# Performance work log

Hardware: AMD Instinct MI355X
Metric: run time of the kernel (lower is better)

## Reference

```python
import jax, jax.numpy as jnp
import numpy as np

N, F_IN, D_OUT, H = 8192, 512, 64, 8
ALPHA = 0.2
NEG_INF = jnp.float32(-9e15)


def setup_inputs() -> dict:
    key = jax.random.key(0)
    k1, k2, k3, k4, k5 = jax.random.split(key, 5)
    x = jax.random.normal(k1, (N, F_IN), dtype=jnp.float32)
    # sparse-ish binary adjacency (avg degree ~33) with self-loops, stored dense
    adj = (jax.random.uniform(k2, (N, N)) < 0.004).astype(jnp.float32)
    adj = jnp.maximum(adj, jnp.eye(N, dtype=jnp.float32))
    W = jax.random.normal(k3, (H, F_IN, D_OUT), dtype=jnp.float32) * 0.05
    a1 = jax.random.normal(k4, (H, D_OUT), dtype=jnp.float32) * 0.05
    a2 = jax.random.normal(k5, (H, D_OUT), dtype=jnp.float32) * 0.05
    return {"x": x, "adj": adj, "W": W, "a1": a1, "a2": a2}


def reference(x, adj, W, a1, a2):
    mask = adj > 0
    outputs = []
    for h in range(H):  # fixed small head count (matches original per-head loop)
        Wh = x @ W[h]                      # [N, D]
        f1 = Wh @ a1[h]                    # [N]
        f2 = Wh @ a2[h]                    # [N]
        e = jax.nn.leaky_relu(f1[:, None] + f2[None, :], ALPHA)  # [N, N]
        att = jnp.where(mask, e, NEG_INF)
        att = jax.nn.softmax(att, axis=1)  # dropout omitted (eval mode)
        outputs.append(att @ Wh)           # [N, D]
    return jnp.concatenate(outputs, axis=1)  # [N, H*D]
```

## Files before the change

kernel.cpp:

```cpp
#include <hip/hip_runtime.h>
#include <hip/hip_bf16.h>
#include <cstdint>

#define N_NODES 8192
#define F_IN    512
#define D_O     64
#define H_N     8
#define NOUT    512
#define MAXD    512

typedef __attribute__((ext_vector_type(8))) short short8;
typedef __attribute__((ext_vector_type(4))) float f32x4;

static __device__ __forceinline__ ushort f2bf(float f) {
  union { float f; uint32_t u; } v; v.f = f;
  uint32_t r = v.u + 0x7FFFu + ((v.u >> 16) & 1u);
  return (ushort)(r >> 16);
}
static __device__ __forceinline__ float bf2f(ushort u) {
  union { uint32_t u; float f; } v; v.u = ((uint32_t)u) << 16;
  return v.f;
}

__global__ __launch_bounds__(256) void convert(const float* __restrict__ x,
                                               const float* __restrict__ W,
                                               ushort* __restrict__ xb,
                                               ushort* __restrict__ Wt) {
  const int gid    = blockIdx.x * 256 + threadIdx.x;
  const int stride = gridDim.x * 256;
  const int NQ = N_NODES * F_IN / 4;
  for (int q = gid; q < NQ; q += stride) {
    const float4 v = ((const float4*)x)[q];
    ushort4 u;
    u.x = f2bf(v.x); u.y = f2bf(v.y); u.z = f2bf(v.z); u.w = f2bf(v.w);
    ((ushort4*)xb)[q] = u;
  }
  const int NW = H_N * D_O * F_IN;
  for (int t = gid; t < NW; t += stride) {
    const int h = t >> 15, rem = t & 32767;
    const int d = rem >> 9, k = rem & 511;
    Wt[t] = f2bf(W[(size_t)h * F_IN * D_O + (size_t)k * D_O + d]);
  }
}

__global__ __launch_bounds__(256) void gemm_xw(const ushort* __restrict__ xb,
                                               const ushort* __restrict__ Wt,
                                               ushort* __restrict__ Whb) {
  __shared__ ushort As[128][40];
  __shared__ ushort Bs[128][40];

  const int tid  = threadIdx.x;
  const int lane = tid & 63;
  const int wv   = tid >> 6;
  const int wr   = wv >> 1, wc = wv & 1;
  const int r0   = blockIdx.y * 128;
  const int c0   = blockIdx.x * 128;
  const int lm   = lane & 15;
  const int lk   = (lane >> 4) * 8;

  f32x4 acc[4][4];
  #pragma unroll
  for (int m2 = 0; m2 < 4; ++m2)
    #pragma unroll
    for (int n2 = 0; n2 < 4; ++n2)
      acc[m2][n2] = (f32x4){0.f, 0.f, 0.f, 0.f};

  for (int k0 = 0; k0 < F_IN; k0 += 32) {
    __syncthreads();
    #pragma unroll
    for (int half = 0; half < 2; ++half) {
      const int cid = half * 256 + tid;
      const int row = cid >> 2, ck = (cid & 3) * 8;
      *(short8*)&As[row][ck] = *(const short8*)&xb[(size_t)(r0 + row) * F_IN + k0 + ck];
      *(short8*)&Bs[row][ck] = *(const short8*)&Wt[(size_t)(c0 + row) * F_IN + k0 + ck];
    }
    __syncthreads();

    short8 af[4], bf[4];
    #pragma unroll
    for (int m2 = 0; m2 < 4; ++m2)
      af[m2] = *(const short8*)&As[wr * 64 + m2 * 16 + lm][lk];
    #pragma unroll
    for (int n2 = 0; n2 < 4; ++n2)
      bf[n2] = *(const short8*)&Bs[wc * 64 + n2 * 16 + lm][lk];
    #pragma unroll
    for (int m2 = 0; m2 < 4; ++m2)
      #pragma unroll
      for (int n2 = 0; n2 < 4; ++n2)
        acc[m2][n2] = __builtin_amdgcn_mfma_f32_16x16x32_bf16(af[m2], bf[n2], acc[m2][n2], 0, 0, 0);
  }

  const int rowb = (lane >> 4) * 4;
  #pragma unroll
  for (int m2 = 0; m2 < 4; ++m2) {
    #pragma unroll
    for (int n2 = 0; n2 < 4; ++n2) {
      const int c     = c0 + wc * 64 + n2 * 16 + lm;
      const int rbase = r0 + wr * 64 + m2 * 16 + rowb;
      #pragma unroll
      for (int r = 0; r < 4; ++r)
        Whb[(size_t)(rbase + r) * NOUT + c] = f2bf(acc[m2][n2][r]);
    }
  }
}

__global__ __launch_bounds__(256) void f_proj(const ushort* __restrict__ Whb,
                                              const float* __restrict__ a1,
                                              const float* __restrict__ a2,
                                              float* __restrict__ f1,
                                              float* __restrict__ f2) {
  const int gw   = blockIdx.x * 4 + (threadIdx.x >> 6);
  const int lane = threadIdx.x & 63;
  const int i = gw >> 3, h = gw & 7;
  const float wv = bf2f(Whb[(size_t)i * NOUT + h * D_O + lane]);
  float v1 = wv * a1[h * D_O + lane];
  float v2 = wv * a2[h * D_O + lane];
  #pragma unroll
  for (int o = 32; o; o >>= 1) {
    v1 += __shfl_xor(v1, o);
    v2 += __shfl_xor(v2, o);
  }
  if (lane == 0) { f1[gw] = v1; f2[gw] = v2; }
}

__global__ __launch_bounds__(256) void gat_attn(const uint32_t* __restrict__ adj,
                                                const ushort* __restrict__ Whb,
                                                const float* __restrict__ f1,
                                                const float* __restrict__ f2,
                                                float* __restrict__ out) {
  const int i    = blockIdx.x;
  const int tid  = threadIdx.x;
  const int lane = tid & 63;
  const int w    = tid >> 6;

  __shared__ int   nbr[MAXD];
  __shared__ float p[MAXD][9];
  __shared__ float f1s[8], invs[8];
  __shared__ int   wsum[4];

  if (tid < 8) f1s[tid] = f1[(size_t)i * H_N + tid];

  const uint32_t* arow = adj + (size_t)i * N_NODES;
  uint32_t bits = 0;
  #pragma unroll
  for (int u = 0; u < 8; ++u) {
    const uint4 a = *(const uint4*)&arow[(u * 256 + tid) * 4];
    if (a.x) bits |= 1u << (u * 4 + 0);
    if (a.y) bits |= 1u << (u * 4 + 1);
    if (a.z) bits |= 1u << (u * 4 + 2);
    if (a.w) bits |= 1u << (u * 4 + 3);
  }
  const int cnt = __popc(bits);
  int v = cnt;
  #pragma unroll
  for (int o = 1; o < 64; o <<= 1) {
    int u = __shfl_up(v, o);
    if (lane >= o) v += u;
  }
  if (lane == 63) wsum[w] = v;
  __syncthreads();
  int base = 0, total = 0;
  #pragma unroll
  for (int ww = 0; ww < 4; ++ww) {
    int s = wsum[ww];
    if (ww < w) base += s;
    total += s;
  }
  const int deg = min(total, MAXD);
  int off = base + v - cnt;
  #pragma unroll
  for (int u = 0; u < 8; ++u)
    #pragma unroll
    for (int b = 0; b < 4; ++b)
      if (bits & (1u << (u * 4 + b))) {
        if (off < MAXD) nbr[off] = (u * 256 + tid) * 4 + b;
        ++off;
      }
  __syncthreads();

  for (int idx = tid; idx < deg * H_N; idx += 256) {
    const int n = idx >> 3, h = idx & 7;
    const int j = nbr[n];
    float l = f1s[h] + f2[(size_t)j * H_N + h];
    l = l > 0.f ? l : 0.2f * l;
    p[n][h] = l;
  }
  __syncthreads();

  #pragma unroll
  for (int hh = 0; hh < 2; ++hh) {
    const int h = w + hh * 4;
    float m = -3.0e38f;
    for (int n = lane; n < deg; n += 64) m = fmaxf(m, p[n][h]);
    #pragma unroll
    for (int o = 32; o; o >>= 1) m = fmaxf(m, __shfl_xor(m, o));
    float s = 0.f;
    for (int n = lane; n < deg; n += 64) {
      const float e = __expf(p[n][h] - m);
      p[n][h] = e;
      s += e;
    }
    #pragma unroll
    for (int o = 32; o; o >>= 1) s += __shfl_xor(s, o);
    if (lane == 0) invs[h] = 1.0f / s;
  }
  __syncthreads();

  const int h = tid >> 5;
  float acc0 = 0.f, acc1 = 0.f;
  #pragma unroll 4
  for (int n = 0; n < deg; ++n) {
    const float pv = p[n][h];
    const ushort2 u = *(const ushort2*)&Whb[(size_t)nbr[n] * NOUT + tid * 2];
    acc0 += pv * bf2f(u.x);
    acc1 += pv * bf2f(u.y);
  }
  const float inv = invs[h];
  float2 o2; o2.x = acc0 * inv; o2.y = acc1 * inv;
  *(float2*)&out[(size_t)i * NOUT + tid * 2] = o2;
}

extern "C" void kernel_launch(void* const* d_in, const int* in_sizes, int n_in,
                              void* d_out, int out_size, void* d_ws, size_t ws_size,
                              hipStream_t stream) {
  const float* x   = (const float*)d_in[0];
  const float* adj = (const float*)d_in[1];
  const float* W   = (const float*)d_in[2];
  const float* a1  = (const float*)d_in[3];
  const float* a2  = (const float*)d_in[4];
  float* out = (float*)d_out;

  ushort* Whb = (ushort*)d_ws;
  ushort* xb  = Whb + (size_t)N_NODES * NOUT;
  ushort* Wt  = xb + (size_t)N_NODES * F_IN;
  float*  f1  = (float*)(Wt + (size_t)H_N * D_O * F_IN);
  float*  f2  = f1 + (size_t)N_NODES * H_N;

  hipLaunchKernelGGL(convert, dim3(2048), dim3(256), 0, stream, x, W, xb, Wt);
  hipLaunchKernelGGL(gemm_xw, dim3(NOUT / 128, N_NODES / 128), dim3(256), 0, stream,
                     xb, Wt, Whb);
  hipLaunchKernelGGL(f_proj, dim3(N_NODES * H_N / 4), dim3(256), 0, stream,
                     Whb, a1, a2, f1, f2);
  hipLaunchKernelGGL(gat_attn, dim3(N_NODES), dim3(256), 0, stream,
                     (const uint32_t*)adj, Whb, f1, f2, out);
}
```

Baseline: 111.0 us.

## Fuse attention projections into GEMM epilogue and tile the W transpose

Folds the f1/f2 projection into the x·W GEMM epilogue, reducing each head's 64 accumulator columns with shuffles, so the separate f_proj kernel and its re-read of Wh disappear. The GEMM tiling becomes 64x128 with BK=64, which doubles the number of blocks. The W transpose in the convert kernel now goes through shared memory so its global reads are coalesced, and a larger unroll is applied to the gather loop in gat_attn. The trade-offs are a heavier epilogue and smaller tiles, which give less reuse per block.

New measurement: 98.28 us. -11.5%, faster.

```diff
diff --git a/kernel.cpp b/kernel.cpp
--- a/kernel.cpp
+++ b/kernel.cpp
@@ -9,6 +9,10 @@
 #define NOUT    512
 #define MAXD    512
 
+#define BM 64
+#define BN 128
+#define BK 64
+
 typedef __attribute__((ext_vector_type(8))) short short8;
 typedef __attribute__((ext_vector_type(4))) float f32x4;
 
@@ -26,101 +30,127 @@
                                                const float* __restrict__ W,
                                                ushort* __restrict__ xb,
                                                ushort* __restrict__ Wt) {
-  const int gid    = blockIdx.x * 256 + threadIdx.x;
-  const int stride = gridDim.x * 256;
-  const int NQ = N_NODES * F_IN / 4;
-  for (int q = gid; q < NQ; q += stride) {
-    const float4 v = ((const float4*)x)[q];
-    ushort4 u;
-    u.x = f2bf(v.x); u.y = f2bf(v.y); u.z = f2bf(v.z); u.w = f2bf(v.w);
-    ((ushort4*)xb)[q] = u;
-  }
-  const int NW = H_N * D_O * F_IN;
-  for (int t = gid; t < NW; t += stride) {
-    const int h = t >> 15, rem = t & 32767;
-    const int d = rem >> 9, k = rem & 511;
-    Wt[t] = f2bf(W[(size_t)h * F_IN * D_O + (size_t)k * D_O + d]);
-  }
-}
-
-__global__ __launch_bounds__(256) void gemm_xw(const ushort* __restrict__ xb,
-                                               const ushort* __restrict__ Wt,
-                                               ushort* __restrict__ Whb) {
-  __shared__ ushort As[128][40];
-  __shared__ ushort Bs[128][40];
+  __shared__ float Ws[64][65];
+  const int b = blockIdx.x, t = threadIdx.x;
+  if (b < 2048) {
+    const int gid = b * 256 + t;
+    #pragma unroll
+    for (int it = 0; it < 2; ++it) {
+      const int q = gid + it * 524288;
+      const float4 v = ((const float4*)x)[q];
+      ushort4 u;
+      u.x = f2bf(v.x); u.y = f2bf(v.y); u.z = f2bf(v.z); u.w = f2bf(v.w);
+      ((ushort4*)xb)[q] = u;
+    }
+  } else {
+    const int bb = b - 2048;
+    const int h = bb >> 3, kt = bb & 7;
+    const int d = t & 63, krg = (t >> 6) * 16;
+    const float* src = &W[((size_t)h * F_IN + kt * 64 + krg) * D_O + d];
+    #pragma unroll
+    for (int q = 0; q < 16; ++q)
+      Ws[krg + q][d] = src[(size_t)q * D_O];
+    __syncthreads();
+    const int d0 = t >> 2, kq = (t & 3) * 16;
+    ushort* dst = &Wt[(size_t)h * D_O * F_IN + (size_t)d0 * F_IN + kt * 64 + kq];
+    #pragma unroll
+    for (int q = 0; q < 16; ++q)
+      dst[q] = f2bf(Ws[kq + q][d0]);
+  }
+}
+
+__global__ __launch_bounds__(256) void gemm_f(const ushort* __restrict__ xb,
+                                              const ushort* __restrict__ Wt,
+                                              const float* __restrict__ a1,
+                                              const float* __restrict__ a2,
+                                              ushort* __restrict__ Whb,
+                                              float* __restrict__ f1,
+                                              float* __restrict__ f2) {
+  __shared__ ushort As[BM][BK + 8];
+  __shared__ ushort Bs[BN][BK + 8];
 
   const int tid  = threadIdx.x;
   const int lane = tid & 63;
   const int wv   = tid >> 6;
   const int wr   = wv >> 1, wc = wv & 1;
-  const int r0   = blockIdx.y * 128;
-  const int c0   = blockIdx.x * 128;
+  const int r0   = blockIdx.y * BM;
+  const int c0   = blockIdx.x * BN;
   const int lm   = lane & 15;
-  const int lk   = (lane >> 4) * 8;
-
-  f32x4 acc[4][4];
-  #pragma unroll
-  for (int m2 = 0; m2 < 4; ++m2)
+  const int lg   = lane >> 4;
+
+  f32x4 acc[2][4];
+  #pragma unroll
+  for (int m2 = 0; m2 < 2; ++m2)
     #pragma unroll
     for (int n2 = 0; n2 < 4; ++n2)
       acc[m2][n2] = (f32x4){0.f, 0.f, 0.f, 0.f};
 
-  for (int k0 = 0; k0 < F_IN; k0 += 32) {
+  for (int k0 = 0; k0 < F_IN; k0 += BK) {
     __syncthreads();
     #pragma unroll
-    for (int half = 0; half < 2; ++half) {
-      const int cid = half * 256 + tid;
-      const int row = cid >> 2, ck = (cid & 3) * 8;
+    for (int p = 0; p < 2; ++p) {
+      const int e = p * 256 + tid;
+      const int row = e >> 3, ck = (e & 7) * 8;
       *(short8*)&As[row][ck] = *(const short8*)&xb[(size_t)(r0 + row) * F_IN + k0 + ck];
+    }
+    #pragma unroll
+    for (int p = 0; p < 4; ++p) {
+      const int e = p * 256 + tid;
+      const int row = e >> 3, ck = (e & 7) * 8;
       *(short8*)&Bs[row][ck] = *(const short8*)&Wt[(size_t)(c0 + row) * F_IN + k0 + ck];
     }
     __syncthreads();
 
-    short8 af[4], bf[4];
-    #pragma unroll
-    for (int m2 = 0; m2 < 4; ++m2)
-      af[m2] = *(const short8*)&As[wr * 64 + m2 * 16 + lm][lk];
-    #pragma unroll
-    for (int n2 = 0; n2 < 4; ++n2)
-      bf[n2] = *(const short8*)&Bs[wc * 64 + n2 * 16 + lm][lk];
-    #pragma unroll
-    for (int m2 = 0; m2 < 4; ++m2)
+    #pragma unroll
+    for (int kk = 0; kk < 2; ++kk) {
+      const int koff = kk * 32 + lg * 8;
+      short8 af[2], bf[4];
+      #pragma unroll
+      for (int m2 = 0; m2 < 2; ++m2)
+        af[m2] = *(const short8*)&As[wr * 32 + m2 * 16 + lm][koff];
       #pragma unroll
       for (int n2 = 0; n2 < 4; ++n2)
-        acc[m2][n2] = __builtin_amdgcn_mfma_f32_16x16x32_bf16(af[m2], bf[n2], acc[m2][n2], 0, 0, 0);
-  }
-
-  const int rowb = (lane >> 4) * 4;
-  #pragma unroll
-  for (int m2 = 0; m2 < 4; ++m2) {
-    #pragma unroll
-    for (int n2 = 0; n2 < 4; ++n2) {
-      const int c     = c0 + wc * 64 + n2 * 16 + lm;
-      const int rbase = r0 + wr * 64 + m2 * 16 + rowb;
-      #pragma unroll
-      for (int r = 0; r < 4; ++r)
-        Whb[(size_t)(rbase + r) * NOUT + c] = f2bf(acc[m2][n2][r]);
-    }
-  }
-}
-
-__global__ __launch_bounds__(256) void f_proj(const ushort* __restrict__ Whb,
-                                              const float* __restrict__ a1,
-                                              const float* __restrict__ a2,
-                                              float* __restrict__ f1,
-                                              float* __restrict__ f2) {
-  const int gw   = blockIdx.x * 4 + (threadIdx.x >> 6);
-  const int lane = threadIdx.x & 63;
-  const int i = gw >> 3, h = gw & 7;
-  const float wv = bf2f(Whb[(size_t)i * NOUT + h * D_O + lane]);
-  float v1 = wv * a1[h * D_O + lane];
-  float v2 = wv * a2[h * D_O + lane];
-  #pragma unroll
-  for (int o = 32; o; o >>= 1) {
-    v1 += __shfl_xor(v1, o);
-    v2 += __shfl_xor(v2, o);
-  }
-  if (lane == 0) { f1[gw] = v1; f2[gw] = v2; }
+        bf[n2] = *(const short8*)&Bs[wc * 64 + n2 * 16 + lm][koff];
+      #pragma unroll
+      for (int m2 = 0; m2 < 2; ++m2)
+        #pragma unroll
+        for (int n2 = 0; n2 < 4; ++n2)
+          acc[m2][n2] = __builtin_amdgcn_mfma_f32_16x16x32_bf16(af[m2], bf[n2], acc[m2][n2], 0, 0, 0);
+    }
+  }
+
+  const int head = (c0 >> 6) + wc;
+  float a1v[4], a2v[4];
+  #pragma unroll
+  for (int n2 = 0; n2 < 4; ++n2) {
+    a1v[n2] = a1[head * D_O + n2 * 16 + lm];
+    a2v[n2] = a2[head * D_O + n2 * 16 + lm];
+  }
+
+  #pragma unroll
+  for (int m2 = 0; m2 < 2; ++m2) {
+    #pragma unroll
+    for (int r = 0; r < 4; ++r) {
+      const int row = r0 + wr * 32 + m2 * 16 + lg * 4 + r;
+      float p1 = 0.f, p2 = 0.f;
+      #pragma unroll
+      for (int n2 = 0; n2 < 4; ++n2) {
+        const float v = acc[m2][n2][r];
+        p1 += v * a1v[n2];
+        p2 += v * a2v[n2];
+        Whb[(size_t)row * NOUT + c0 + wc * 64 + n2 * 16 + lm] = f2bf(v);
+      }
+      #pragma unroll
+      for (int o = 1; o < 16; o <<= 1) {
+        p1 += __shfl_xor(p1, o);
+        p2 += __shfl_xor(p2, o);
+      }
+      if (lm == 0) {
+        f1[(size_t)row * H_N + head] = p1;
+        f2[(size_t)row * H_N + head] = p2;
+      }
+    }
+  }
 }
 
 __global__ __launch_bounds__(256) void gat_attn(const uint32_t* __restrict__ adj,
@@ -171,9 +201,9 @@
   #pragma unroll
   for (int u = 0; u < 8; ++u)
     #pragma unroll
-    for (int b = 0; b < 4; ++b)
-      if (bits & (1u << (u * 4 + b))) {
-        if (off < MAXD) nbr[off] = (u * 256 + tid) * 4 + b;
+    for (int bq = 0; bq < 4; ++bq)
+      if (bits & (1u << (u * 4 + bq))) {
+        if (off < MAXD) nbr[off] = (u * 256 + tid) * 4 + bq;
         ++off;
       }
   __syncthreads();
@@ -208,7 +238,7 @@
 
   const int h = tid >> 5;
   float acc0 = 0.f, acc1 = 0.f;
-  #pragma unroll 4
+  #pragma unroll 8
   for (int n = 0; n < deg; ++n) {
     const float pv = p[n][h];
     const ushort2 u = *(const ushort2*)&Whb[(size_t)nbr[n] * NOUT + tid * 2];
@@ -236,11 +266,9 @@
   float*  f1  = (float*)(Wt + (size_t)H_N * D_O * F_IN);
   float*  f2  = f1 + (size_t)N_NODES * H_N;
 
-  hipLaunchKernelGGL(convert, dim3(2048), dim3(256), 0, stream, x, W, xb, Wt);
-  hipLaunchKernelGGL(gemm_xw, dim3(NOUT / 128, N_NODES / 128), dim3(256), 0, stream,
-                     xb, Wt, Whb);
-  hipLaunchKernelGGL(f_proj, dim3(N_NODES * H_N / 4), dim3(256), 0, stream,
-                     Whb, a1, a2, f1, f2);
+  hipLaunchKernelGGL(convert, dim3(2112), dim3(256), 0, stream, x, W, xb, Wt);
+  hipLaunchKernelGGL(gemm_f, dim3(NOUT / BN, N_NODES / BM), dim3(256), 0, stream,
+                     xb, Wt, a1, a2, Whb, f1, f2);
   hipLaunchKernelGGL(gat_attn, dim3(N_NODES), dim3(256), 0, stream,
                      (const uint32_t*)adj, Whb, f1, f2, out);
 }
```
